# Optimization experiments

Hardware: AMD Instinct MI355X
Metric: run time of the kernel (lower is better)

## Reference

```python
import jax, jax.numpy as jnp
import numpy as np

N = 10000       # nodes
E = 640000      # edges (before self-loops)
D_IN = 128
H1 = 128
H2 = 64
EMB = 64
NEG_SLOPE = 0.2  # PyG GATConv default


def setup_inputs() -> dict:
    key = jax.random.key(0)
    ks = jax.random.split(key, 12)
    s = 0.05
    return {
        "x": jax.random.normal(ks[0], (N, D_IN), dtype=jnp.float32),
        "edge_index": jax.random.randint(ks[1], (2, E), 0, N, dtype=jnp.int64),
        "W1": jax.random.normal(ks[2], (D_IN, H1), dtype=jnp.float32) * s,
        "a_src1": jax.random.normal(ks[3], (H1,), dtype=jnp.float32) * s,
        "a_dst1": jax.random.normal(ks[4], (H1,), dtype=jnp.float32) * s,
        "b1": jnp.zeros((H1,), dtype=jnp.float32),
        "W2": jax.random.normal(ks[5], (H1, H2), dtype=jnp.float32) * s,
        "a_src2": jax.random.normal(ks[6], (H2,), dtype=jnp.float32) * s,
        "a_dst2": jax.random.normal(ks[7], (H2,), dtype=jnp.float32) * s,
        "b2": jnp.zeros((H2,), dtype=jnp.float32),
        "Wp": jax.random.normal(ks[8], (H2, EMB), dtype=jnp.float32) * s,
        "bp": jnp.zeros((EMB,), dtype=jnp.float32),
    }


def _gat_conv(x, src, dst, W, a_src, a_dst, b):
    # x: [N, Din] -> h: [N, Dout]
    h = x @ W
    # edge-wise attention logits (PyG: alpha_src from source j, alpha_dst from target i)
    logits = jax.nn.leaky_relu((h @ a_src)[src] + (h @ a_dst)[dst], NEG_SLOPE)  # [E+N]
    # softmax over incoming edges of each destination node (numerically stable)
    m = jax.ops.segment_max(logits, dst, num_segments=N)
    e = jnp.exp(logits - m[dst])
    z = jax.ops.segment_sum(e, dst, num_segments=N)
    w = e / z[dst]                                                              # [E+N]
    # weighted scatter-add of source features into destinations
    out = jax.ops.segment_sum(w[:, None] * h[src], dst, num_segments=N)         # [N, Dout]
    return out + b


def reference(x, edge_index, W1, a_src1, a_dst1, b1, W2, a_src2, a_dst2, b2, Wp, bp):
    # add self-loops (PyG GATConv default add_self_loops=True)
    loop = jnp.arange(N, dtype=edge_index.dtype)
    ei = jnp.concatenate([edge_index, jnp.stack([loop, loop])], axis=1)
    src, dst = ei[0], ei[1]
    x1 = jax.nn.relu(_gat_conv(x, src, dst, W1, a_src1, a_dst1, b1))
    x2 = jax.nn.relu(_gat_conv(x1, src, dst, W2, a_src2, a_dst2, b2))
    return x2 @ Wp + bp  # [N, EMB]
```

## Files before the change

### kernel.cpp

```cpp
#include <hip/hip_runtime.h>
#include <hip/hip_bf16.h>

#define NNODES 10000
#define NEDGES 640000
#define NTOT   (NNODES + NEDGES)
#define D_IN 128
#define H1 128
#define H2 64
#define EMB 64

#define NBUCKET 160
#define BCAP    8192
#define CHUNK   4096
#define NCHUNK  ((NTOT + CHUNK - 1) / CHUNK)
#define NTILE   ((NNODES + 31) / 32)

typedef _Float16 half2v __attribute__((ext_vector_type(2)));
typedef _Float16 half4v __attribute__((ext_vector_type(4)));

union SMemA {
    struct { int ordered[CHUNK]; int hist[NBUCKET]; int binStart[NBUCKET];
             int bincur[NBUCKET]; int gcur[NBUCKET]; int wtmp[4]; } p1;
    struct { float A[32 * 64]; float B[64 * 128]; } g;
};

__device__ __forceinline__ void bucket_chunk(SMemA& sm, int c, const int* __restrict__ ei,
                                             int* __restrict__ bucket_cursor,
                                             int* __restrict__ bucket_arr) {
    int tid = threadIdx.x;
    int base = c * CHUNK;
    int n = NTOT - base; if (n > CHUNK) n = CHUNK;

    int rec[CHUNK / 256];
#pragma unroll
    for (int k = 0; k < CHUNK / 256; ++k) {
        int i = base + k * 256 + tid;
        int r = 0;
        if (i < NTOT) {
            int s, d;
            if (i < NEDGES) { s = ei[i]; d = ei[NEDGES + i]; }
            else            { s = d = i - NEDGES; }
            r = (d << 16) | s;
        }
        rec[k] = r;
    }

    for (int b = tid; b < NBUCKET; b += 256) sm.p1.hist[b] = 0;
    __syncthreads();
#pragma unroll
    for (int k = 0; k < CHUNK / 256; ++k) {
        int i = base + k * 256 + tid;
        if (i < NTOT) atomicAdd(&sm.p1.hist[rec[k] >> 22], 1);
    }
    __syncthreads();

    {
        int v = (tid < NBUCKET) ? sm.p1.hist[tid] : 0;
        int lane = tid & 63, w = tid >> 6;
        int inc = v;
        for (int o = 1; o < 64; o <<= 1) {
            int t = __shfl_up(inc, o, 64);
            if (lane >= o) inc += t;
        }
        if (lane == 63) sm.p1.wtmp[w] = inc;
        __syncthreads();
        int pre = 0;
        for (int i = 0; i < w; ++i) pre += sm.p1.wtmp[i];
        if (tid < NBUCKET) {
            sm.p1.binStart[tid] = pre + inc - v;
            sm.p1.bincur[tid]   = pre + inc - v;
        }
    }
    __syncthreads();

#pragma unroll
    for (int k = 0; k < CHUNK / 256; ++k) {
        int i = base + k * 256 + tid;
        if (i < NTOT) {
            int pos = atomicAdd(&sm.p1.bincur[rec[k] >> 22], 1);
            sm.p1.ordered[pos] = rec[k];
        }
    }
    __syncthreads();

    for (int b = tid; b < NBUCKET; b += 256) {
        int cc = sm.p1.hist[b];
        sm.p1.gcur[b] = cc ? atomicAdd(&bucket_cursor[b], cc) : 0;
    }
    __syncthreads();

#pragma unroll
    for (int k = 0; k < CHUNK / 256; ++k) {
        int i = k * 256 + tid;
        if (i < n) {
            int r = sm.p1.ordered[i];
            int b = r >> 22;
            bucket_arr[b * BCAP + sm.p1.gcur[b] + (i - sm.p1.binStart[b])] = r;
        }
    }
}

__device__ __forceinline__ void gemm1_tile(SMemA& sm, int t,
                                           const float* __restrict__ x,
                                           const float* __restrict__ W1,
                                           const float* __restrict__ a_src1,
                                           const float* __restrict__ a_dst1,
                                           _Float16* __restrict__ h1h,
                                           float* __restrict__ as1,
                                           float* __restrict__ ad1) {
    int tid = threadIdx.x;
    int row0 = t * 32;
    int tx = tid & 31;
    int ty = tid >> 5;
    float acc[4][4];
#pragma unroll
    for (int rr = 0; rr < 4; ++rr)
#pragma unroll
        for (int cc = 0; cc < 4; ++cc) acc[rr][cc] = 0.f;

    for (int kk = 0; kk < D_IN; kk += 64) {
        float4* Al4 = (float4*)sm.g.A;
        for (int idx = tid; idx < 32 * 16; idx += 256) {
            int r = idx >> 4, c = idx & 15;
            float4 z4 = {0.f, 0.f, 0.f, 0.f};
            Al4[idx] = (row0 + r < NNODES)
                ? ((const float4*)(x + (size_t)(row0 + r) * D_IN + kk))[c] : z4;
        }
        float4* Bl4 = (float4*)sm.g.B;
        const float4* B4 = (const float4*)(W1 + (size_t)kk * H1);
        for (int idx = tid; idx < 64 * H1 / 4; idx += 256) Bl4[idx] = B4[idx];
        __syncthreads();

        for (int k = 0; k < 64; ++k) {
            float bv[4];
            const float* Bk = &sm.g.B[k * H1 + tx * 4];
#pragma unroll
            for (int cc = 0; cc < 4; ++cc) bv[cc] = Bk[cc];
#pragma unroll
            for (int rr = 0; rr < 4; ++rr) {
                float a = sm.g.A[(ty + 8 * rr) * 64 + k];
#pragma unroll
                for (int cc = 0; cc < 4; ++cc) acc[rr][cc] = fmaf(a, bv[cc], acc[rr][cc]);
            }
        }
        __syncthreads();
    }

#pragma unroll
    for (int rr = 0; rr < 4; ++rr) {
        int gr = row0 + ty + 8 * rr;
        if (gr < NNODES) {
            half4v hv;
            hv.x = (_Float16)acc[rr][0]; hv.y = (_Float16)acc[rr][1];
            hv.z = (_Float16)acc[rr][2]; hv.w = (_Float16)acc[rr][3];
            ((half4v*)(h1h + (size_t)gr * H1))[tx] = hv;
        }
    }

    float asv[4], adv[4];
#pragma unroll
    for (int cc = 0; cc < 4; ++cc) {
        asv[cc] = a_src1[tx * 4 + cc];
        adv[cc] = a_dst1[tx * 4 + cc];
    }
#pragma unroll
    for (int rr = 0; rr < 4; ++rr) {
        float s1 = 0.f, s2 = 0.f;
#pragma unroll
        for (int cc = 0; cc < 4; ++cc) {
            s1 = fmaf(acc[rr][cc], asv[cc], s1);
            s2 = fmaf(acc[rr][cc], adv[cc], s2);
        }
#pragma unroll
        for (int o = 1; o < 32; o <<= 1) {
            s1 += __shfl_xor(s1, o, 64);
            s2 += __shfl_xor(s2, o, 64);
        }
        int gr = row0 + ty + 8 * rr;
        if (tx == 0 && gr < NNODES) { as1[gr] = s1; ad1[gr] = s2; }
    }
}

__global__ __launch_bounds__(256) void csr_gemm1_kernel(const int* __restrict__ ei,
                                                        int* __restrict__ bucket_cursor,
                                                        int* __restrict__ bucket_arr,
                                                        const float* __restrict__ x,
                                                        const float* __restrict__ W1,
                                                        const float* __restrict__ a_src1,
                                                        const float* __restrict__ a_dst1,
                                                        _Float16* __restrict__ h1h,
                                                        float* __restrict__ as1,
                                                        float* __restrict__ ad1) {
    __shared__ SMemA sm;
    int bid = blockIdx.x;
    if (bid < NCHUNK)
        bucket_chunk(sm, bid, ei, bucket_cursor, bucket_arr);
    else
        gemm1_tile(sm, bid - NCHUNK, x, W1, a_src1, a_dst1, h1h, as1, ad1);
}

__global__ __launch_bounds__(256) void build_kernel(const int* __restrict__ bucket_cursor,
                                                    const int* __restrict__ bucket_arr,
                                                    int* __restrict__ rowptr,
                                                    int* __restrict__ csr_src) {
    __shared__ int sbase[NBUCKET];
    __shared__ int wtmp[4];
    __shared__ int hist[64];
    __shared__ int bincur[64];
    int tid = threadIdx.x;
    int b = blockIdx.x;

    {
        int v = (tid < NBUCKET) ? bucket_cursor[tid] : 0;
        int lane = tid & 63, w = tid >> 6;
        int inc = v;
        for (int o = 1; o < 64; o <<= 1) {
            int t = __shfl_up(inc, o, 64);
            if (lane >= o) inc += t;
        }
        if (lane == 63) wtmp[w] = inc;
        __syncthreads();
        int pre = 0;
        for (int i = 0; i < w; ++i) pre += wtmp[i];
        if (tid < NBUCKET) sbase[tid] = pre + inc - v;
    }
    __syncthreads();

    int cnt = bucket_cursor[b];
    int base = sbase[b];
    const int* arr = bucket_arr + b * BCAP;

    if (tid < 64) hist[tid] = 0;
    __syncthreads();
    for (int i = tid; i < cnt; i += 256) atomicAdd(&hist[(arr[i] >> 16) & 63], 1);
    __syncthreads();

    if (tid < 64) {
        int v = hist[tid];
        int inc = v;
        for (int o = 1; o < 64; o <<= 1) {
            int t = __shfl_up(inc, o, 64);
            if (tid >= o) inc += t;
        }
        bincur[tid] = inc - v;
        int node = b * 64 + tid;
        if (node < NNODES) rowptr[node] = base + inc - v;
    }
    if (b == 0 && tid == 0) rowptr[NNODES] = NTOT;
    __syncthreads();

    for (int i = tid; i < cnt; i += 256) {
        int r = arr[i];
        int pos = base + atomicAdd(&bincur[(r >> 16) & 63], 1);
        csr_src[pos] = r & 0xFFFF;
    }
}

__global__ __launch_bounds__(256) void agg1_gemm2_kernel(const int* __restrict__ rowptr,
                                                         const int* __restrict__ csr_src,
                                                         const _Float16* __restrict__ h1h,
                                                         const float* __restrict__ as1,
                                                         const float* __restrict__ ad1,
                                                         const float* __restrict__ b1,
                                                         const float* __restrict__ W2,
                                                         const float* __restrict__ a_src2,
                                                         const float* __restrict__ a_dst2,
                                                         _Float16* __restrict__ h2h,
                                                         float* __restrict__ as2,
                                                         float* __restrict__ ad2) {
    __shared__ float Wlds[H1 * H2];
    __shared__ float xrow[4][H1];
    int tid = threadIdx.x;
    {
        const float4* W4 = (const float4*)W2;
        float4* Wl4 = (float4*)Wlds;
        for (int idx = tid; idx < H1 * H2 / 4; idx += 256) Wl4[idx] = W4[idx];
    }
    int wv = tid >> 6, lane = tid & 63;
    int wid = blockIdx.x * 4 + wv;
    int beg = rowptr[wid], end = rowptr[wid + 1];
    float ad_d = ad1[wid];
    float z = 0.f, acc0 = 0.f, acc1 = 0.f;
    const half2v* h1p = (const half2v*)h1h;

    for (int chunk = beg; chunk < end; chunk += 64) {
        int myj = chunk + lane;
        int cnt = end - chunk; if (cnt > 64) cnt = 64;
        int s_l = 0; float e_l = 0.f;
        if (myj < end) {
            s_l = csr_src[myj];
            float l = as1[s_l] + ad_d;
            l = (l > 0.f) ? l : 0.2f * l;
            e_l = __expf(l);
        }
        z += e_l;
        int cnt8 = (cnt + 7) & ~7;
        for (int t = 0; t < cnt8; t += 8) {
#pragma unroll
            for (int u = 0; u < 8; ++u) {
                int tt = __builtin_amdgcn_readfirstlane(t + u);
                int s = __builtin_amdgcn_readlane(s_l, tt);
                float e = __int_as_float(
                    __builtin_amdgcn_readlane(__float_as_int(e_l), tt));
                half2v hp = h1p[(size_t)s * 64 + lane];
                acc0 = fmaf(e, (float)hp.x, acc0);
                acc1 = fmaf(e, (float)hp.y, acc1);
            }
        }
    }
    for (int o = 32; o; o >>= 1) z += __shfl_xor(z, o, 64);
    float rz = 1.f / z;
    float2 bb = ((const float2*)b1)[lane];
    float v0 = fmaxf(acc0 * rz + bb.x, 0.f);
    float v1 = fmaxf(acc1 * rz + bb.y, 0.f);
    ((float2*)xrow[wv])[lane] = make_float2(v0, v1);
    __syncthreads();

    float hacc = 0.f;
    const float* xr = xrow[wv];
    for (int k = 0; k < H1; k += 4) {
        float4 xq = *(const float4*)&xr[k];
        hacc = fmaf(xq.x, Wlds[(k + 0) * H2 + lane], hacc);
        hacc = fmaf(xq.y, Wlds[(k + 1) * H2 + lane], hacc);
        hacc = fmaf(xq.z, Wlds[(k + 2) * H2 + lane], hacc);
        hacc = fmaf(xq.w, Wlds[(k + 3) * H2 + lane], hacc);
    }
    float s1 = hacc * a_src2[lane];
    float s2 = hacc * a_dst2[lane];
    for (int o = 32; o; o >>= 1) {
        s1 += __shfl_xor(s1, o, 64);
        s2 += __shfl_xor(s2, o, 64);
    }
    if (lane == 0) { as2[wid] = s1; ad2[wid] = s2; }
    h2h[(size_t)wid * H2 + lane] = (_Float16)hacc;
}

__global__ __launch_bounds__(256) void agg2_proj_kernel(const int* __restrict__ rowptr,
                                                        const int* __restrict__ csr_src,
                                                        const _Float16* __restrict__ h2h,
                                                        const float* __restrict__ as2,
                                                        const float* __restrict__ ad2,
                                                        const float* __restrict__ b2,
                                                        const float* __restrict__ Wp,
                                                        const float* __restrict__ bp,
                                                        float* __restrict__ out) {
    __shared__ float Wlds[H2 * EMB];
    __shared__ float xrow[4][H2];
    int tid = threadIdx.x;
    {
        const float4* W4 = (const float4*)Wp;
        float4* Wl4 = (float4*)Wlds;
        for (int idx = tid; idx < H2 * EMB / 4; idx += 256) Wl4[idx] = W4[idx];
    }
    int wv = tid >> 6, lane = tid & 63;
    int wid = blockIdx.x * 4 + wv;
    int beg = rowptr[wid], end = rowptr[wid + 1];
    float ad_d = ad2[wid];
    float z = 0.f, acc = 0.f;

    for (int chunk = beg; chunk < end; chunk += 64) {
        int myj = chunk + lane;
        int cnt = end - chunk; if (cnt > 64) cnt = 64;
        int s_l = 0; float e_l = 0.f;
        if (myj < end) {
            s_l = csr_src[myj];
            float l = as2[s_l] + ad_d;
            l = (l > 0.f) ? l : 0.2f * l;
            e_l = __expf(l);
        }
        z += e_l;
        int cnt8 = (cnt + 7) & ~7;
        for (int t = 0; t < cnt8; t += 8) {
#pragma unroll
            for (int u = 0; u < 8; ++u) {
                int tt = __builtin_amdgcn_readfirstlane(t + u);
                int s = __builtin_amdgcn_readlane(s_l, tt);
                float e = __int_as_float(
                    __builtin_amdgcn_readlane(__float_as_int(e_l), tt));
                acc = fmaf(e, (float)h2h[(size_t)s * H2 + lane], acc);
            }
        }
    }
    for (int o = 32; o; o >>= 1) z += __shfl_xor(z, o, 64);
    float x2v = fmaxf(acc * (1.f / z) + b2[lane], 0.f);
    xrow[wv][lane] = x2v;
    __syncthreads();

    float oacc = 0.f;
    const float* xr = xrow[wv];
    for (int k = 0; k < H2; k += 4) {
        float4 xq = *(const float4*)&xr[k];
        oacc = fmaf(xq.x, Wlds[(k + 0) * EMB + lane], oacc);
        oacc = fmaf(xq.y, Wlds[(k + 1) * EMB + lane], oacc);
        oacc = fmaf(xq.z, Wlds[(k + 2) * EMB + lane], oacc);
        oacc = fmaf(xq.w, Wlds[(k + 3) * EMB + lane], oacc);
    }
    out[(size_t)wid * EMB + lane] = oacc + bp[lane];
}


extern "C" void kernel_launch(void* const* d_in, const int* in_sizes, int n_in,
                              void* d_out, int out_size, void* d_ws, size_t ws_size,
                              hipStream_t stream) {
    const float* x      = (const float*)d_in[0];
    const int*   ei     = (const int*)d_in[1];
    const float* W1     = (const float*)d_in[2];
    const float* a_src1 = (const float*)d_in[3];
    const float* a_dst1 = (const float*)d_in[4];
    const float* b1     = (const float*)d_in[5];
    const float* W2     = (const float*)d_in[6];
    const float* a_src2 = (const float*)d_in[7];
    const float* a_dst2 = (const float*)d_in[8];
    const float* b2     = (const float*)d_in[9];
    const float* Wp     = (const float*)d_in[10];
    const float* bp     = (const float*)d_in[11];
    float* out = (float*)d_out;

    char* ws = (char*)d_ws;
    size_t off = 0;
    auto alloc = [&](size_t bytes) {
        void* p = ws + off;
        off = (off + bytes + 255) & ~(size_t)255;
        return p;
    };
    int*      bucket_cursor = (int*)alloc(NBUCKET * 4);
    int*      bucket_arr    = (int*)alloc((size_t)NBUCKET * BCAP * 4);
    int*      rowptr  = (int*)alloc((NNODES + 1) * 4);
    int*      csr_src = (int*)alloc((size_t)NTOT * 4);
    _Float16* h1h     = (_Float16*)alloc((size_t)NNODES * H1 * 2);
    float*    as1     = (float*)alloc(NNODES * 4);
    float*    ad1     = (float*)alloc(NNODES * 4);
    _Float16* h2h     = (_Float16*)alloc((size_t)NNODES * H2 * 2);
    float*    as2     = (float*)alloc(NNODES * 4);
    float*    ad2     = (float*)alloc(NNODES * 4);
    (void)ws_size;

    const int TB = 256;
    int wave_b = NNODES / 4;

    hipMemsetAsync(bucket_cursor, 0, NBUCKET * 4, stream);

    csr_gemm1_kernel<<<NCHUNK + NTILE, TB, 0, stream>>>(
        ei, bucket_cursor, bucket_arr, x, W1, a_src1, a_dst1, h1h, as1, ad1);

    build_kernel<<<(NNODES + 63) / 64, TB, 0, stream>>>(bucket_cursor,
                                                        bucket_arr, rowptr, csr_src);

    agg1_gemm2_kernel<<<wave_b, TB, 0, stream>>>(rowptr, csr_src, h1h, as1, ad1,
                                                 b1, W2, a_src2, a_dst2,
                                                 h2h, as2, ad2);

    agg2_proj_kernel<<<wave_b, TB, 0, stream>>>(rowptr, csr_src, h2h, as2, ad2,
                                                b2, Wp, bp, out);
}
```

Before: 162.9 us.

## Fuse all GAT stages into one persistent kernel with grid-wide barriers

Merges the bucketing/GEMM1, CSR build, layer-1 aggregation plus GEMM2, and layer-2 aggregation plus projection kernels into a single persistent launch of 768 blocks. Stages are separated by atomic-counter grid barriers, and work is distributed with grid-stride loops. The GEMM1 k-tile is shrunk to 32 so the shared-memory union fits four blocks per CU. This removes per-kernel launch and drain gaps. In exchange it relies on every block being co-resident for the spin barriers and adds barrier spin latency.

```diff
diff --git a/kernel.cpp b/kernel.cpp
--- a/kernel.cpp
+++ b/kernel.cpp
@@ -14,17 +14,34 @@
 #define CHUNK   4096
 #define NCHUNK  ((NTOT + CHUNK - 1) / CHUNK)
 #define NTILE   ((NNODES + 31) / 32)
+#define NBBLK   ((NNODES + 63) / 64)
+#define GRID    768
+#define TB      256
+#define NWAVES  (GRID * 4)
 
 typedef _Float16 half2v __attribute__((ext_vector_type(2)));
 typedef _Float16 half4v __attribute__((ext_vector_type(4)));
 
-union SMemA {
+union SMem {
     struct { int ordered[CHUNK]; int hist[NBUCKET]; int binStart[NBUCKET];
              int bincur[NBUCKET]; int gcur[NBUCKET]; int wtmp[4]; } p1;
-    struct { float A[32 * 64]; float B[64 * 128]; } g;
+    struct { int sbase[NBUCKET]; int wtmp[4]; int hist[64]; int bincur[64]; } p2;
+    struct { float A[32 * 32]; float B[32 * 128]; } g1;
+    struct { float W[H1 * H2]; float xrow[4][H1]; } c;
+    struct { float W[H2 * EMB]; float xrow[4][H2]; } d;
 };
 
-__device__ __forceinline__ void bucket_chunk(SMemA& sm, int c, const int* __restrict__ ei,
+__device__ __forceinline__ void gridbar(int* __restrict__ bar, int k) {
+    __syncthreads();
+    if (threadIdx.x == 0) {
+        __hip_atomic_fetch_add(&bar[k], 1, __ATOMIC_RELEASE, __HIP_MEMORY_SCOPE_AGENT);
+        while (__hip_atomic_load(&bar[k], __ATOMIC_ACQUIRE, __HIP_MEMORY_SCOPE_AGENT) < GRID)
+            __builtin_amdgcn_s_sleep(2);
+    }
+    __syncthreads();
+}
+
+__device__ __forceinline__ void bucket_chunk(SMem& sm, int c, const int* __restrict__ ei,
                                              int* __restrict__ bucket_cursor,
                                              int* __restrict__ bucket_arr) {
     int tid = threadIdx.x;
@@ -100,7 +117,7 @@
     }
 }
 
-__device__ __forceinline__ void gemm1_tile(SMemA& sm, int t,
+__device__ __forceinline__ void gemm1_tile(SMem& sm, int t,
                                            const float* __restrict__ x,
                                            const float* __restrict__ W1,
                                            const float* __restrict__ a_src1,
@@ -118,29 +135,28 @@
 #pragma unroll
         for (int cc = 0; cc < 4; ++cc) acc[rr][cc] = 0.f;
 
-    for (int kk = 0; kk < D_IN; kk += 64) {
-        float4* Al4 = (float4*)sm.g.A;
-        for (int idx = tid; idx < 32 * 16; idx += 256) {
-            int r = idx >> 4, c = idx & 15;
+    for (int kk = 0; kk < D_IN; kk += 32) {
+        float4* Al4 = (float4*)sm.g1.A;
+        for (int idx = tid; idx < 32 * 8; idx += 256) {
+            int r = idx >> 3, c = idx & 7;
             float4 z4 = {0.f, 0.f, 0.f, 0.f};
             Al4[idx] = (row0 + r < NNODES)
                 ? ((const float4*)(x + (size_t)(row0 + r) * D_IN + kk))[c] : z4;
         }
-        float4* Bl4 = (float4*)sm.g.B;
+        float4* Bl4 = (float4*)sm.g1.B;
         const float4* B4 = (const float4*)(W1 + (size_t)kk * H1);
-        for (int idx = tid; idx < 64 * H1 / 4; idx += 256) Bl4[idx] = B4[idx];
-        __syncthreads();
-
-        for (int k = 0; k < 64; ++k) {
-            float bv[4];
-            const float* Bk = &sm.g.B[k * H1 + tx * 4];
-#pragma unroll
-            for (int cc = 0; cc < 4; ++cc) bv[cc] = Bk[cc];
+        for (int idx = tid; idx < 32 * H1 / 4; idx += 256) Bl4[idx] = B4[idx];
+        __syncthreads();
+
+        for (int k = 0; k < 32; ++k) {
+            float4 bv = *(const float4*)&sm.g1.B[k * H1 + tx * 4];
 #pragma unroll
             for (int rr = 0; rr < 4; ++rr) {
-                float a = sm.g.A[(ty + 8 * rr) * 64 + k];
-#pragma unroll
-                for (int cc = 0; cc < 4; ++cc) acc[rr][cc] = fmaf(a, bv[cc], acc[rr][cc]);
+                float a = sm.g1.A[(ty + 8 * rr) * 32 + k];
+                acc[rr][0] = fmaf(a, bv.x, acc[rr][0]);
+                acc[rr][1] = fmaf(a, bv.y, acc[rr][1]);
+                acc[rr][2] = fmaf(a, bv.z, acc[rr][2]);
+                acc[rr][3] = fmaf(a, bv.w, acc[rr][3]);
             }
         }
         __syncthreads();
@@ -181,35 +197,12 @@
     }
 }
 
-__global__ __launch_bounds__(256) void csr_gemm1_kernel(const int* __restrict__ ei,
-                                                        int* __restrict__ bucket_cursor,
-                                                        int* __restrict__ bucket_arr,
-                                                        const float* __restrict__ x,
-                                                        const float* __restrict__ W1,
-                                                        const float* __restrict__ a_src1,
-                                                        const float* __restrict__ a_dst1,
-                                                        _Float16* __restrict__ h1h,
-                                                        float* __restrict__ as1,
-                                                        float* __restrict__ ad1) {
-    __shared__ SMemA sm;
-    int bid = blockIdx.x;
-    if (bid < NCHUNK)
-        bucket_chunk(sm, bid, ei, bucket_cursor, bucket_arr);
-    else
-        gemm1_tile(sm, bid - NCHUNK, x, W1, a_src1, a_dst1, h1h, as1, ad1);
-}
-
-__global__ __launch_bounds__(256) void build_kernel(const int* __restrict__ bucket_cursor,
-                                                    const int* __restrict__ bucket_arr,
-                                                    int* __restrict__ rowptr,
-                                                    int* __restrict__ csr_src) {
-    __shared__ int sbase[NBUCKET];
-    __shared__ int wtmp[4];
-    __shared__ int hist[64];
-    __shared__ int bincur[64];
+__device__ __forceinline__ void build_bucket(SMem& sm, int b,
+                                             const int* __restrict__ bucket_cursor,
+                                             const int* __restrict__ bucket_arr,
+                                             int* __restrict__ rowptr,
+                                             int* __restrict__ csr_src) {
     int tid = threadIdx.x;
-    int b = blockIdx.x;
-
     {
         int v = (tid < NBUCKET) ? bucket_cursor[tid] : 0;
         int lane = tid & 63, w = tid >> 6;
@@ -218,31 +211,31 @@
             int t = __shfl_up(inc, o, 64);
             if (lane >= o) inc += t;
         }
-        if (lane == 63) wtmp[w] = inc;
+        if (lane == 63) sm.p2.wtmp[w] = inc;
         __syncthreads();
         int pre = 0;
-        for (int i = 0; i < w; ++i) pre += wtmp[i];
-        if (tid < NBUCKET) sbase[tid] = pre + inc - v;
+        for (int i = 0; i < w; ++i) pre += sm.p2.wtmp[i];
+        if (tid < NBUCKET) sm.p2.sbase[tid] = pre + inc - v;
     }
     __syncthreads();
 
     int cnt = bucket_cursor[b];
-    int base = sbase[b];
+    int base = sm.p2.sbase[b];
     const int* arr = bucket_arr + b * BCAP;
 
-    if (tid < 64) hist[tid] = 0;
-    __syncthreads();
-    for (int i = tid; i < cnt; i += 256) atomicAdd(&hist[(arr[i] >> 16) & 63], 1);
+    if (tid < 64) sm.p2.hist[tid] = 0;
+    __syncthreads();
+    for (int i = tid; i < cnt; i += 256) atomicAdd(&sm.p2.hist[(arr[i] >> 16) & 63], 1);
     __syncthreads();
 
     if (tid < 64) {
-        int v = hist[tid];
+        int v = sm.p2.hist[tid];
         int inc = v;
         for (int o = 1; o < 64; o <<= 1) {
             int t = __shfl_up(inc, o, 64);
             if (tid >= o) inc += t;
         }
-        bincur[tid] = inc - v;
+        sm.p2.bincur[tid] = inc - v;
         int node = b * 64 + tid;
         if (node < NNODES) rowptr[node] = base + inc - v;
     }
@@ -251,151 +244,167 @@
 
     for (int i = tid; i < cnt; i += 256) {
         int r = arr[i];
-        int pos = base + atomicAdd(&bincur[(r >> 16) & 63], 1);
+        int pos = base + atomicAdd(&sm.p2.bincur[(r >> 16) & 63], 1);
         csr_src[pos] = r & 0xFFFF;
     }
 }
 
-__global__ __launch_bounds__(256) void agg1_gemm2_kernel(const int* __restrict__ rowptr,
-                                                         const int* __restrict__ csr_src,
-                                                         const _Float16* __restrict__ h1h,
-                                                         const float* __restrict__ as1,
-                                                         const float* __restrict__ ad1,
-                                                         const float* __restrict__ b1,
-                                                         const float* __restrict__ W2,
-                                                         const float* __restrict__ a_src2,
-                                                         const float* __restrict__ a_dst2,
-                                                         _Float16* __restrict__ h2h,
-                                                         float* __restrict__ as2,
-                                                         float* __restrict__ ad2) {
-    __shared__ float Wlds[H1 * H2];
-    __shared__ float xrow[4][H1];
+__global__ __launch_bounds__(TB, 4) void mega(const float* __restrict__ x,
+                                              const int* __restrict__ ei,
+                                              const float* __restrict__ W1,
+                                              const float* __restrict__ a_src1,
+                                              const float* __restrict__ a_dst1,
+                                              const float* __restrict__ b1,
+                                              const float* __restrict__ W2,
+                                              const float* __restrict__ a_src2,
+                                              const float* __restrict__ a_dst2,
+                                              const float* __restrict__ b2,
+                                              const float* __restrict__ Wp,
+                                              const float* __restrict__ bp,
+                                              float* __restrict__ out,
+                                              int* __restrict__ bar,
+                                              int* __restrict__ bucket_cursor,
+                                              int* __restrict__ bucket_arr,
+                                              int* __restrict__ rowptr,
+                                              int* __restrict__ csr_src,
+                                              _Float16* __restrict__ h1h,
+                                              float* __restrict__ as1,
+                                              float* __restrict__ ad1,
+                                              _Float16* __restrict__ h2h,
+                                              float* __restrict__ as2,
+                                              float* __restrict__ ad2) {
+    __shared__ SMem sm;
+    int bid = blockIdx.x;
     int tid = threadIdx.x;
+    int wv = tid >> 6, lane = tid & 63;
+
+    if (bid < NCHUNK) {
+        bucket_chunk(sm, bid, ei, bucket_cursor, bucket_arr);
+    } else {
+        for (int t = bid - NCHUNK; t < NTILE; t += GRID - NCHUNK)
+            gemm1_tile(sm, t, x, W1, a_src1, a_dst1, h1h, as1, ad1);
+    }
+    gridbar(bar, 0);
+
+    if (bid < NBBLK)
+        build_bucket(sm, bid, bucket_cursor, bucket_arr, rowptr, csr_src);
+    gridbar(bar, 1);
+
     {
         const float4* W4 = (const float4*)W2;
-        float4* Wl4 = (float4*)Wlds;
+        float4* Wl4 = (float4*)sm.c.W;
         for (int idx = tid; idx < H1 * H2 / 4; idx += 256) Wl4[idx] = W4[idx];
-    }
-    int wv = tid >> 6, lane = tid & 63;
-    int wid = blockIdx.x * 4 + wv;
-    int beg = rowptr[wid], end = rowptr[wid + 1];
-    float ad_d = ad1[wid];
-    float z = 0.f, acc0 = 0.f, acc1 = 0.f;
-    const half2v* h1p = (const half2v*)h1h;
-
-    for (int chunk = beg; chunk < end; chunk += 64) {
-        int myj = chunk + lane;
-        int cnt = end - chunk; if (cnt > 64) cnt = 64;
-        int s_l = 0; float e_l = 0.f;
-        if (myj < end) {
-            s_l = csr_src[myj];
-            float l = as1[s_l] + ad_d;
-            l = (l > 0.f) ? l : 0.2f * l;
-            e_l = __expf(l);
-        }
-        z += e_l;
-        int cnt8 = (cnt + 7) & ~7;
-        for (int t = 0; t < cnt8; t += 8) {
-#pragma unroll
-            for (int u = 0; u < 8; ++u) {
-                int tt = __builtin_amdgcn_readfirstlane(t + u);
-                int s = __builtin_amdgcn_readlane(s_l, tt);
-                float e = __int_as_float(
-                    __builtin_amdgcn_readlane(__float_as_int(e_l), tt));
-                half2v hp = h1p[(size_t)s * 64 + lane];
-                acc0 = fmaf(e, (float)hp.x, acc0);
-                acc1 = fmaf(e, (float)hp.y, acc1);
-            }
-        }
-    }
-    for (int o = 32; o; o >>= 1) z += __shfl_xor(z, o, 64);
-    float rz = 1.f / z;
-    float2 bb = ((const float2*)b1)[lane];
-    float v0 = fmaxf(acc0 * rz + bb.x, 0.f);
-    float v1 = fmaxf(acc1 * rz + bb.y, 0.f);
-    ((float2*)xrow[wv])[lane] = make_float2(v0, v1);
-    __syncthreads();
-
-    float hacc = 0.f;
-    const float* xr = xrow[wv];
-    for (int k = 0; k < H1; k += 4) {
-        float4 xq = *(const float4*)&xr[k];
-        hacc = fmaf(xq.x, Wlds[(k + 0) * H2 + lane], hacc);
-        hacc = fmaf(xq.y, Wlds[(k + 1) * H2 + lane], hacc);
-        hacc = fmaf(xq.z, Wlds[(k + 2) * H2 + lane], hacc);
-        hacc = fmaf(xq.w, Wlds[(k + 3) * H2 + lane], hacc);
-    }
-    float s1 = hacc * a_src2[lane];
-    float s2 = hacc * a_dst2[lane];
-    for (int o = 32; o; o >>= 1) {
-        s1 += __shfl_xor(s1, o, 64);
-        s2 += __shfl_xor(s2, o, 64);
-    }
-    if (lane == 0) { as2[wid] = s1; ad2[wid] = s2; }
-    h2h[(size_t)wid * H2 + lane] = (_Float16)hacc;
-}
-
-__global__ __launch_bounds__(256) void agg2_proj_kernel(const int* __restrict__ rowptr,
-                                                        const int* __restrict__ csr_src,
-                                                        const _Float16* __restrict__ h2h,
-                                                        const float* __restrict__ as2,
-                                                        const float* __restrict__ ad2,
-                                                        const float* __restrict__ b2,
-                                                        const float* __restrict__ Wp,
-                                                        const float* __restrict__ bp,
-                                                        float* __restrict__ out) {
-    __shared__ float Wlds[H2 * EMB];
-    __shared__ float xrow[4][H2];
-    int tid = threadIdx.x;
+        __syncthreads();
+        const half2v* h1p = (const half2v*)h1h;
+
+        for (int wid = bid * 4 + wv; wid < NNODES; wid += NWAVES) {
+            int beg = rowptr[wid], end = rowptr[wid + 1];
+            float ad_d = ad1[wid];
+            float z = 0.f, acc0 = 0.f, acc1 = 0.f;
+
+            for (int chunk = beg; chunk < end; chunk += 64) {
+                int myj = chunk + lane;
+                int cnt = end - chunk; if (cnt > 64) cnt = 64;
+                int s_l = 0; float e_l = 0.f;
+                if (myj < end) {
+                    s_l = csr_src[myj];
+                    float l = as1[s_l] + ad_d;
+                    l = (l > 0.f) ? l : 0.2f * l;
+                    e_l = __expf(l);
+                }
+                z += e_l;
+                int cnt8 = (cnt + 7) & ~7;
+                for (int t = 0; t < cnt8; t += 8) {
+#pragma unroll
+                    for (int u = 0; u < 8; ++u) {
+                        int tt = __builtin_amdgcn_readfirstlane(t + u);
+                        int s = __builtin_amdgcn_readlane(s_l, tt);
+                        float e = __int_as_float(
+                            __builtin_amdgcn_readlane(__float_as_int(e_l), tt));
+                        half2v hp = h1p[(size_t)s * 64 + lane];
+                        acc0 = fmaf(e, (float)hp.x, acc0);
+                        acc1 = fmaf(e, (float)hp.y, acc1);
+                    }
+                }
+            }
+            for (int o = 32; o; o >>= 1) z += __shfl_xor(z, o, 64);
+            float rz = 1.f / z;
+            float2 bb = ((const float2*)b1)[lane];
+            float v0 = fmaxf(acc0 * rz + bb.x, 0.f);
+            float v1 = fmaxf(acc1 * rz + bb.y, 0.f);
+            ((float2*)sm.c.xrow[wv])[lane] = make_float2(v0, v1);
+
+            float hacc = 0.f;
+            const float* xr = sm.c.xrow[wv];
+            for (int k = 0; k < H1; k += 4) {
+                float4 xq = *(const float4*)&xr[k];
+                hacc = fmaf(xq.x, sm.c.W[(k + 0) * H2 + lane], hacc);
+                hacc = fmaf(xq.y, sm.c.W[(k + 1) * H2 + lane], hacc);
+                hacc = fmaf(xq.z, sm.c.W[(k + 2) * H2 + lane], hacc);
+                hacc = fmaf(xq.w, sm.c.W[(k + 3) * H2 + lane], hacc);
+            }
+            float s1 = hacc * a_src2[lane];
+            float s2 = hacc * a_dst2[lane];
+            for (int o = 32; o; o >>= 1) {
+                s1 += __shfl_xor(s1, o, 64);
+                s2 += __shfl_xor(s2, o, 64);
+            }
+            if (lane == 0) { as2[wid] = s1; ad2[wid] = s2; }
+            h2h[(size_t)wid * H2 + lane] = (_Float16)hacc;
+        }
+    }
+    gridbar(bar, 2);
+
     {
         const float4* W4 = (const float4*)Wp;
-        float4* Wl4 = (float4*)Wlds;
+        float4* Wl4 = (float4*)sm.d.W;
         for (int idx = tid; idx < H2 * EMB / 4; idx += 256) Wl4[idx] = W4[idx];
-    }
-    int wv = tid >> 6, lane = tid & 63;
-    int wid = blockIdx.x * 4 + wv;
-    int beg = rowptr[wid], end = rowptr[wid + 1];
-    float ad_d = ad2[wid];
-    float z = 0.f, acc = 0.f;
-
-    for (int chunk = beg; chunk < end; chunk += 64) {
-        int myj = chunk + lane;
-        int cnt = end - chunk; if (cnt > 64) cnt = 64;
-        int s_l = 0; float e_l = 0.f;
-        if (myj < end) {
-            s_l = csr_src[myj];
-            float l = as2[s_l] + ad_d;
-            l = (l > 0.f) ? l : 0.2f * l;
-            e_l = __expf(l);
-        }
-        z += e_l;
-        int cnt8 = (cnt + 7) & ~7;
-        for (int t = 0; t < cnt8; t += 8) {
-#pragma unroll
-            for (int u = 0; u < 8; ++u) {
-                int tt = __builtin_amdgcn_readfirstlane(t + u);
-                int s = __builtin_amdgcn_readlane(s_l, tt);
-                float e = __int_as_float(
-                    __builtin_amdgcn_readlane(__float_as_int(e_l), tt));
-                acc = fmaf(e, (float)h2h[(size_t)s * H2 + lane], acc);
-            }
-        }
-    }
-    for (int o = 32; o; o >>= 1) z += __shfl_xor(z, o, 64);
-    float x2v = fmaxf(acc * (1.f / z) + b2[lane], 0.f);
-    xrow[wv][lane] = x2v;
-    __syncthreads();
-
-    float oacc = 0.f;
-    const float* xr = xrow[wv];
-    for (int k = 0; k < H2; k += 4) {
-        float4 xq = *(const float4*)&xr[k];
-        oacc = fmaf(xq.x, Wlds[(k + 0) * EMB + lane], oacc);
-        oacc = fmaf(xq.y, Wlds[(k + 1) * EMB + lane], oacc);
-        oacc = fmaf(xq.z, Wlds[(k + 2) * EMB + lane], oacc);
-        oacc = fmaf(xq.w, Wlds[(k + 3) * EMB + lane], oacc);
-    }
-    out[(size_t)wid * EMB + lane] = oacc + bp[lane];
+        __syncthreads();
+
+        for (int wid = bid * 4 + wv; wid < NNODES; wid += NWAVES) {
+            int beg = rowptr[wid], end = rowptr[wid + 1];
+            float ad_d = ad2[wid];
+            float z = 0.f, acc = 0.f;
+
+            for (int chunk = beg; chunk < end; chunk += 64) {
+                int myj = chunk + lane;
+                int cnt = end - chunk; if (cnt > 64) cnt = 64;
+                int s_l = 0; float e_l = 0.f;
+                if (myj < end) {
+                    s_l = csr_src[myj];
+                    float l = as2[s_l] + ad_d;
+                    l = (l > 0.f) ? l : 0.2f * l;
+                    e_l = __expf(l);
+                }
+                z += e_l;
+                int cnt8 = (cnt + 7) & ~7;
+                for (int t = 0; t < cnt8; t += 8) {
+#pragma unroll
+                    for (int u = 0; u < 8; ++u) {
+                        int tt = __builtin_amdgcn_readfirstlane(t + u);
+                        int s = __builtin_amdgcn_readlane(s_l, tt);
+                        float e = __int_as_float(
+                            __builtin_amdgcn_readlane(__float_as_int(e_l), tt));
+                        acc = fmaf(e, (float)h2h[(size_t)s * H2 + lane], acc);
+                    }
+                }
+            }
+            for (int o = 32; o; o >>= 1) z += __shfl_xor(z, o, 64);
+            float x2v = fmaxf(acc * (1.f / z) + b2[lane], 0.f);
+            sm.d.xrow[wv][lane] = x2v;
+
+            float oacc = 0.f;
+            const float* xr = sm.d.xrow[wv];
+            for (int k = 0; k < H2; k += 4) {
+                float4 xq = *(const float4*)&xr[k];
+                oacc = fmaf(xq.x, sm.d.W[(k + 0) * EMB + lane], oacc);
+                oacc = fmaf(xq.y, sm.d.W[(k + 1) * EMB + lane], oacc);
+                oacc = fmaf(xq.z, sm.d.W[(k + 2) * EMB + lane], oacc);
+                oacc = fmaf(xq.w, sm.d.W[(k + 3) * EMB + lane], oacc);
+            }
+            out[(size_t)wid * EMB + lane] = oacc + bp[lane];
+        }
+    }
 }
 
 
@@ -423,7 +432,9 @@
         off = (off + bytes + 255) & ~(size_t)255;
         return p;
     };
+    int*      bar           = (int*)alloc(16 * 4);
     int*      bucket_cursor = (int*)alloc(NBUCKET * 4);
+    size_t zero_bytes = off;
     int*      bucket_arr    = (int*)alloc((size_t)NBUCKET * BCAP * 4);
     int*      rowptr  = (int*)alloc((NNODES + 1) * 4);
     int*      csr_src = (int*)alloc((size_t)NTOT * 4);
@@ -433,23 +444,11 @@
     _Float16* h2h     = (_Float16*)alloc((size_t)NNODES * H2 * 2);
     float*    as2     = (float*)alloc(NNODES * 4);
     float*    ad2     = (float*)alloc(NNODES * 4);
-    (void)ws_size;
-
-    const int TB = 256;
-    int wave_b = NNODES / 4;
-
-    hipMemsetAsync(bucket_cursor, 0, NBUCKET * 4, stream);
-
-    csr_gemm1_kernel<<<NCHUNK + NTILE, TB, 0, stream>>>(
-        ei, bucket_cursor, bucket_arr, x, W1, a_src1, a_dst1, h1h, as1, ad1);
-
-    build_kernel<<<(NNODES + 63) / 64, TB, 0, stream>>>(bucket_cursor,
-                                                        bucket_arr, rowptr, csr_src);
-
-    agg1_gemm2_kernel<<<wave_b, TB, 0, stream>>>(rowptr, csr_src, h1h, as1, ad1,
-                                                 b1, W2, a_src2, a_dst2,
-                                                 h2h, as2, ad2);
-
-    agg2_proj_kernel<<<wave_b, TB, 0, stream>>>(rowptr, csr_src, h2h, as2, ad2,
-                                                b2, Wp, bp, out);
-}
+    (void)ws_size; (void)in_sizes; (void)n_in; (void)out_size;
+
+    hipMemsetAsync(d_ws, 0, zero_bytes, stream);
+    mega<<<GRID, TB, 0, stream>>>(x, ei, W1, a_src1, a_dst1, b1,
+                                  W2, a_src2, a_dst2, b2, Wp, bp, out,
+                                  bar, bucket_cursor, bucket_arr, rowptr, csr_src,
+                                  h1h, as1, ad1, h2h, as2, ad2);
+}
```

Result: slower. 591.4 us (+263.1%).
